# Kernel tuning notes

Hardware: AMD Instinct MI355X
Metric: run time of the kernel (lower is better)

The kernel has to match this reference:

```python
import jax, jax.numpy as jnp
import numpy as np

HID = 1024  # hidden size of the bilinear interaction space

def setup_inputs() -> dict:
    key = jax.random.key(0)
    k1, k2, kw1, kb1, kw2, kwo, kbo = jax.random.split(key, 7)
    B, N1, N2, D1, D2, OUT = 4, 128, 128, 768, 768, 2
    s1 = 1.0 / np.sqrt(D1)
    s2 = 1.0 / np.sqrt(D2)
    so = 1.0 / np.sqrt(HID)
    return {
        "input1": jax.random.normal(k1, (B, N1, D1), dtype=jnp.float32),
        "input2": jax.random.normal(k2, (B, N2, D2), dtype=jnp.float32),
        # torch nn.Linear convention: weight [out, in], y = x @ W.T + b
        "W1": jax.random.uniform(kw1, (HID, D1), jnp.float32, -s1, s1),
        "b1": jax.random.uniform(kb1, (HID,), jnp.float32, -s1, s1),
        "W2": jax.random.uniform(kw2, (HID, D2), jnp.float32, -s2, s2),  # bias=False
        "Wo": jax.random.uniform(kwo, (OUT, HID), jnp.float32, -so, so),
        "bo": jax.random.uniform(kbo, (OUT,), jnp.float32, -so, so),
    }

def reference(input1, input2, W1, b1, W2, Wo, bo):
    # in1: [B, N1, HID], in2: [B, N2, HID]
    in1 = jnp.einsum("bnd,hd->bnh", input1, W1) + b1
    in2 = jnp.einsum("bmd,hd->bmh", input2, W2)
    # broadcast outer-sum -> [B, N1, N2, HID], ReLU, then project to OUT
    h = jax.nn.relu(in1[:, :, None, :] + in2[:, None, :, :])
    return jnp.einsum("bnmh,oh->bnmo", h, Wo) + bo
```

## Files before the change

kernel.cpp:

```cpp
#include <hip/hip_runtime.h>
#include <hip/hip_bf16.h>


typedef __attribute__((ext_vector_type(8))) short s16x8;
typedef __attribute__((ext_vector_type(4))) float f32x4;

#define KP 2304
#define BK 64
#define KHALF 1152
#define NSTEP (KHALF / BK)

__device__ __forceinline__ void gl_lds16(const void* g, void* l) {
    __builtin_amdgcn_global_load_lds(
        (const __attribute__((address_space(1))) unsigned int*)g,
        (__attribute__((address_space(3))) unsigned int*)l, 16, 0, 0);
}

__global__ __launch_bounds__(256) void prepack(
    const float* __restrict__ in1, const float* __restrict__ in2,
    const float* __restrict__ W1, const float* __restrict__ W2,
    ushort* __restrict__ Abig, ushort* __restrict__ Wbig)
{
    const int gid = blockIdx.x * 256 + threadIdx.x;
    const int src = gid / 196608;
    const int rem = gid % 196608;
    const int row = rem / 192;
    const int k4  = (rem % 192) * 4;
    const float* sp;
    ushort* dst;
    if (src == 0) {
        sp  = (row < 512) ? in1 + (size_t)row * 768 + k4
                          : in2 + (size_t)(row - 512) * 768 + k4;
        dst = Abig + (size_t)row * KP + k4;
    } else {
        sp  = (src == 1 ? W1 : W2) + (size_t)row * 768 + k4;
        dst = Wbig + (size_t)(src - 1) * (1024 * KP) + (size_t)row * KP + k4;
    }
    const float4 x = *(const float4*)sp;
    const float xf[4] = {x.x, x.y, x.z, x.w};
    ushort h[4], l[4];
    #pragma unroll
    for (int i = 0; i < 4; ++i) {
        const float v = xf[i];
        __hip_bfloat16 bh = __float2bfloat16(v);
        const float fh = __bfloat162float(bh);
        __hip_bfloat16 bl = __float2bfloat16(v - fh);
        h[i] = *(ushort*)&bh;
        l[i] = *(ushort*)&bl;
    }
    const ushort4 H = make_ushort4(h[0], h[1], h[2], h[3]);
    const ushort4 L = make_ushort4(l[0], l[1], l[2], l[3]);
    if (src == 0) {
        *(ushort4*)(dst)        = H;
        *(ushort4*)(dst + 768)  = L;
        *(ushort4*)(dst + 1536) = H;
    } else {
        *(ushort4*)(dst)        = H;
        *(ushort4*)(dst + 768)  = H;
        *(ushort4*)(dst + 1536) = L;
    }
}

__global__ __launch_bounds__(512) void gemm_mfma(
    const ushort* __restrict__ Abig, const ushort* __restrict__ Wbig,
    const float* __restrict__ b1, float* __restrict__ hid)
{
    const int t    = threadIdx.x;
    const int lane = t & 63;
    const int w    = t >> 6;
    const int kh   = w >> 2;
    const int ws   = w & 3;
    const int row0 = blockIdx.y * 64;
    const int col0 = blockIdx.x * 64;

    const char* __restrict__ A = (const char*)(Abig + (size_t)row0 * KP);
    const char* __restrict__ W = (const char*)(Wbig
                                   + (row0 < 512 ? (size_t)0 : (size_t)1024 * KP)
                                   + (size_t)col0 * KP);

    __shared__ ushort lds[2][2][2][4096];

    const int srow = t >> 3;
    const int kbyt = (((t & 7) ^ (srow & 7)) << 4);
    const size_t rowoff = (size_t)srow * (KP * 2);

    const int wr = ws >> 1, wc = ws & 1;
    const int l15 = lane & 15, kg = lane >> 4;
    int aoff[2][2], boff[2][2];
    #pragma unroll
    for (int kk = 0; kk < 2; ++kk)
        #pragma unroll
        for (int f = 0; f < 2; ++f) {
            const int r = wr * 32 + f * 16 + l15;
            const int c = wc * 32 + f * 16 + l15;
            const int sw_ = kk * 64 + kg * 16;
            aoff[kk][f] = r * 128 + (sw_ ^ ((r & 7) << 4));
            boff[kk][f] = c * 128 + (sw_ ^ ((c & 7) << 4));
        }

#define STAGE(buf, ktk) do {                                                   \
        const size_t kby = (size_t)(ktk) * (BK * 2);                           \
        _Pragma("unroll")                                                      \
        for (int p = 0; p < 4; ++p) {                                          \
            const char* src = (p & 1) ? W : A;                                 \
            const size_t off = rowoff + (size_t)(p >> 1) * (KHALF * 2)         \
                               + kby + kbyt;                                   \
            gl_lds16(src + off,                                                \
                     (char*)&lds[buf][p >> 1][p & 1][0] + t * 16);             \
        }                                                                      \
    } while (0)

    const f32x4 zero = {0.f, 0.f, 0.f, 0.f};
    f32x4 acc[2][2] = {{zero, zero}, {zero, zero}};

    STAGE(0, 0);
    int cur = 0;
    for (int kt = 0; kt < NSTEP; ++kt) {
        asm volatile("s_waitcnt vmcnt(0)" ::: "memory");
        __syncthreads();
        if (kt + 1 < NSTEP) STAGE(cur ^ 1, kt + 1);
        const char* __restrict__ ab = (const char*)&lds[cur][kh][0][0];
        const char* __restrict__ wb = (const char*)&lds[cur][kh][1][0];
        #pragma unroll
        for (int kk = 0; kk < 2; ++kk) {
            s16x8 af[2], bf_[2];
            #pragma unroll
            for (int f = 0; f < 2; ++f) {
                af[f]  = *(const s16x8*)(ab + aoff[kk][f]);
                bf_[f] = *(const s16x8*)(wb + boff[kk][f]);
            }
            #pragma unroll
            for (int fr = 0; fr < 2; ++fr)
                #pragma unroll
                for (int fc = 0; fc < 2; ++fc)
                    acc[fr][fc] = __builtin_amdgcn_mfma_f32_16x16x32_bf16(
                        af[fr], bf_[fc], acc[fr][fc], 0, 0, 0);
        }
        cur ^= 1;
    }
#undef STAGE

    __syncthreads();
    float* red = (float*)&lds[0][0][0][0];
    if (kh == 1) {
        #pragma unroll
        for (int fr = 0; fr < 2; ++fr)
            #pragma unroll
            for (int fc = 0; fc < 2; ++fc)
                *(f32x4*)&red[(((ws * 2 + fr) * 2 + fc) * 64 + lane) * 4] =
                    acc[fr][fc];
    }
    __syncthreads();
    if (kh == 0) {
        float bias[2] = {0.f, 0.f};
        if (row0 < 512) {
            bias[0] = b1[col0 + wc * 32 + l15];
            bias[1] = b1[col0 + wc * 32 + 16 + l15];
        }
        #pragma unroll
        for (int fr = 0; fr < 2; ++fr)
            #pragma unroll
            for (int fc = 0; fc < 2; ++fc) {
                const f32x4 o = *(const f32x4*)
                    &red[(((ws * 2 + fr) * 2 + fc) * 64 + lane) * 4];
                #pragma unroll
                for (int i = 0; i < 4; ++i) {
                    const int r = row0 + wr * 32 + fr * 16 + kg * 4 + i;
                    const int c = col0 + wc * 32 + fc * 16 + l15;
                    hid[(size_t)r * 1024 + c] = acc[fr][fc][i] + o[i] + bias[fc];
                }
            }
    }
}

__global__ __launch_bounds__(256) void pair_kernel(
    const float* __restrict__ hid, const float* __restrict__ Wo,
    const float* __restrict__ bo, float* __restrict__ out)
{
    const int t  = threadIdx.x;
    const int b  = blockIdx.z;
    const int n0 = blockIdx.y * 16;
    const int m0 = blockIdx.x * 16;

    __shared__ float s1[2][16][132];
    __shared__ float s2[2][16][132];
    __shared__ float sw[2][1024];

    #pragma unroll
    for (int q = 0; q < 2; ++q) {
        const int fi = q * 256 + t;
        ((float4*)sw)[fi] = ((const float4*)Wo)[fi];
    }

    const int rr0 = t >> 5;
    const int cc  = (t & 31) << 2;
    const float* __restrict__ base1 = hid + ((size_t)(b * 128 + n0)) * 1024;
    const float* __restrict__ base2 = hid + ((size_t)(512 + b * 128 + m0)) * 1024;

    float4 a0 = *(const float4*)&base1[(size_t)rr0 * 1024 + cc];
    float4 a1 = *(const float4*)&base1[(size_t)(rr0 + 8) * 1024 + cc];
    float4 c0 = *(const float4*)&base2[(size_t)rr0 * 1024 + cc];
    float4 c1 = *(const float4*)&base2[(size_t)(rr0 + 8) * 1024 + cc];

    const int i = t >> 4, j = t & 15;
    float acc0 = 0.f, acc1 = 0.f;
    int cur = 0;

    for (int hc = 0; hc < 8; ++hc) {
        *(float4*)&s1[cur][rr0][cc]     = a0;
        *(float4*)&s1[cur][rr0 + 8][cc] = a1;
        *(float4*)&s2[cur][rr0][cc]     = c0;
        *(float4*)&s2[cur][rr0 + 8][cc] = c1;
        __syncthreads();
        if (hc < 7) {
            const int off = (hc + 1) * 128 + cc;
            a0 = *(const float4*)&base1[(size_t)rr0 * 1024 + off];
            a1 = *(const float4*)&base1[(size_t)(rr0 + 8) * 1024 + off];
            c0 = *(const float4*)&base2[(size_t)rr0 * 1024 + off];
            c1 = *(const float4*)&base2[(size_t)(rr0 + 8) * 1024 + off];
        }
        const float* __restrict__ xrow = &s1[cur][i][0];
        const float* __restrict__ yrow = &s2[cur][j][0];
        const float* __restrict__ u = &sw[0][hc * 128];
        const float* __restrict__ v = &sw[1][hc * 128];
        #pragma unroll
        for (int c4 = 0; c4 < 32; ++c4) {
            const float4 x = *(const float4*)&xrow[c4 * 4];
            const float4 y = *(const float4*)&yrow[c4 * 4];
            const float4 uu = *(const float4*)&u[c4 * 4];
            const float4 vv = *(const float4*)&v[c4 * 4];
            float r;
            r = fmaxf(x.x + y.x, 0.f); acc0 = fmaf(r, uu.x, acc0); acc1 = fmaf(r, vv.x, acc1);
            r = fmaxf(x.y + y.y, 0.f); acc0 = fmaf(r, uu.y, acc0); acc1 = fmaf(r, vv.y, acc1);
            r = fmaxf(x.z + y.z, 0.f); acc0 = fmaf(r, uu.z, acc0); acc1 = fmaf(r, vv.z, acc1);
            r = fmaxf(x.w + y.w, 0.f); acc0 = fmaf(r, uu.w, acc0); acc1 = fmaf(r, vv.w, acc1);
        }
        __syncthreads();
        cur ^= 1;
    }

    const float2 ob = *(const float2*)bo;
    const size_t P = (((size_t)b * 128 + n0 + i) * 128 + (m0 + j)) * 2;
    *(float2*)&out[P] = make_float2(acc0 + ob.x, acc1 + ob.y);
}

extern "C" void kernel_launch(void* const* d_in, const int* in_sizes, int n_in,
                              void* d_out, int out_size, void* d_ws, size_t ws_size,
                              hipStream_t stream) {
    (void)in_sizes; (void)n_in; (void)out_size; (void)ws_size;
    const float* input1 = (const float*)d_in[0];
    const float* input2 = (const float*)d_in[1];
    const float* W1     = (const float*)d_in[2];
    const float* b1     = (const float*)d_in[3];
    const float* W2     = (const float*)d_in[4];
    const float* Wo     = (const float*)d_in[5];
    const float* bo     = (const float*)d_in[6];
    float* out = (float*)d_out;

    ushort* Abig = (ushort*)d_ws;
    ushort* Wbig = Abig + (size_t)1024 * KP;
    float*  hid  = (float*)(Wbig + (size_t)2 * 1024 * KP);

    prepack<<<2304, 256, 0, stream>>>(input1, input2, W1, W2, Abig, Wbig);
    gemm_mfma<<<dim3(16, 16), 512, 0, stream>>>(Abig, Wbig, b1, hid);
    pair_kernel<<<dim3(8, 8, 4), 256, 0, stream>>>(hid, Wo, bo, out);
}
```

Before: 109.2 us.

## Split pair kernel over hidden dimension with atomic accumulation for more blocks

```diff
diff --git a/kernel.cpp b/kernel.cpp
--- a/kernel.cpp
+++ b/kernel.cpp
@@ -173,75 +173,66 @@
     }
 }
 
+__global__ __launch_bounds__(256) void out_init(
+    const float* __restrict__ bo, float* __restrict__ out)
+{
+    const int g = blockIdx.x * 256 + threadIdx.x;
+    *(float2*)&out[(size_t)g * 2] = make_float2(bo[0], bo[1]);
+}
+
 __global__ __launch_bounds__(256) void pair_kernel(
     const float* __restrict__ hid, const float* __restrict__ Wo,
-    const float* __restrict__ bo, float* __restrict__ out)
+    float* __restrict__ out)
 {
     const int t  = threadIdx.x;
-    const int b  = blockIdx.z;
+    const int b  = blockIdx.z >> 2;
+    const int h0 = (blockIdx.z & 3) * 256;
     const int n0 = blockIdx.y * 16;
     const int m0 = blockIdx.x * 16;
 
-    __shared__ float s1[2][16][132];
-    __shared__ float s2[2][16][132];
-    __shared__ float sw[2][1024];
+    __shared__ float s1[16][260];
+    __shared__ float s2[16][260];
+    __shared__ float sw[2][256];
+
+    const float* __restrict__ base1 = hid + ((size_t)(b * 128 + n0)) * 1024 + h0;
+    const float* __restrict__ base2 = hid + ((size_t)(512 + b * 128 + m0)) * 1024 + h0;
 
     #pragma unroll
-    for (int q = 0; q < 2; ++q) {
-        const int fi = q * 256 + t;
-        ((float4*)sw)[fi] = ((const float4*)Wo)[fi];
-    }
-
-    const int rr0 = t >> 5;
-    const int cc  = (t & 31) << 2;
-    const float* __restrict__ base1 = hid + ((size_t)(b * 128 + n0)) * 1024;
-    const float* __restrict__ base2 = hid + ((size_t)(512 + b * 128 + m0)) * 1024;
-
-    float4 a0 = *(const float4*)&base1[(size_t)rr0 * 1024 + cc];
-    float4 a1 = *(const float4*)&base1[(size_t)(rr0 + 8) * 1024 + cc];
-    float4 c0 = *(const float4*)&base2[(size_t)rr0 * 1024 + cc];
-    float4 c1 = *(const float4*)&base2[(size_t)(rr0 + 8) * 1024 + cc];
+    for (int p = 0; p < 4; ++p) {
+        const int slot = p * 256 + t;
+        const int r  = slot >> 6;
+        const int c  = (slot & 63) << 2;
+        *(float4*)&s1[r][c] = *(const float4*)&base1[(size_t)r * 1024 + c];
+        *(float4*)&s2[r][c] = *(const float4*)&base2[(size_t)r * 1024 + c];
+    }
+    if (t < 128) {
+        const int o = t >> 6;
+        const int c = (t & 63) << 2;
+        *(float4*)&sw[o][c] = *(const float4*)&Wo[(size_t)o * 1024 + h0 + c];
+    }
+    __syncthreads();
 
     const int i = t >> 4, j = t & 15;
+    const float* __restrict__ xrow = &s1[i][0];
+    const float* __restrict__ yrow = &s2[j][0];
     float acc0 = 0.f, acc1 = 0.f;
-    int cur = 0;
-
-    for (int hc = 0; hc < 8; ++hc) {
-        *(float4*)&s1[cur][rr0][cc]     = a0;
-        *(float4*)&s1[cur][rr0 + 8][cc] = a1;
-        *(float4*)&s2[cur][rr0][cc]     = c0;
-        *(float4*)&s2[cur][rr0 + 8][cc] = c1;
-        __syncthreads();
-        if (hc < 7) {
-            const int off = (hc + 1) * 128 + cc;
-            a0 = *(const float4*)&base1[(size_t)rr0 * 1024 + off];
-            a1 = *(const float4*)&base1[(size_t)(rr0 + 8) * 1024 + off];
-            c0 = *(const float4*)&base2[(size_t)rr0 * 1024 + off];
-            c1 = *(const float4*)&base2[(size_t)(rr0 + 8) * 1024 + off];
-        }
-        const float* __restrict__ xrow = &s1[cur][i][0];
-        const float* __restrict__ yrow = &s2[cur][j][0];
-        const float* __restrict__ u = &sw[0][hc * 128];
-        const float* __restrict__ v = &sw[1][hc * 128];
-        #pragma unroll
-        for (int c4 = 0; c4 < 32; ++c4) {
-            const float4 x = *(const float4*)&xrow[c4 * 4];
-            const float4 y = *(const float4*)&yrow[c4 * 4];
-            const float4 uu = *(const float4*)&u[c4 * 4];
-            const float4 vv = *(const float4*)&v[c4 * 4];
-            float r;
-            r = fmaxf(x.x + y.x, 0.f); acc0 = fmaf(r, uu.x, acc0); acc1 = fmaf(r, vv.x, acc1);
-            r = fmaxf(x.y + y.y, 0.f); acc0 = fmaf(r, uu.y, acc0); acc1 = fmaf(r, vv.y, acc1);
-            r = fmaxf(x.z + y.z, 0.f); acc0 = fmaf(r, uu.z, acc0); acc1 = fmaf(r, vv.z, acc1);
-            r = fmaxf(x.w + y.w, 0.f); acc0 = fmaf(r, uu.w, acc0); acc1 = fmaf(r, vv.w, acc1);
-        }
-        __syncthreads();
-        cur ^= 1;
-    }
-
-    const float2 ob = *(const float2*)bo;
+
+    #pragma unroll 8
+    for (int c4 = 0; c4 < 64; ++c4) {
+        const float4 x  = *(const float4*)&xrow[c4 * 4];
+        const float4 y  = *(const float4*)&yrow[c4 * 4];
+        const float4 uu = *(const float4*)&sw[0][c4 * 4];
+        const float4 vv = *(const float4*)&sw[1][c4 * 4];
+        float r;
+        r = fmaxf(x.x + y.x, 0.f); acc0 = fmaf(r, uu.x, acc0); acc1 = fmaf(r, vv.x, acc1);
+        r = fmaxf(x.y + y.y, 0.f); acc0 = fmaf(r, uu.y, acc0); acc1 = fmaf(r, vv.y, acc1);
+        r = fmaxf(x.z + y.z, 0.f); acc0 = fmaf(r, uu.z, acc0); acc1 = fmaf(r, vv.z, acc1);
+        r = fmaxf(x.w + y.w, 0.f); acc0 = fmaf(r, uu.w, acc0); acc1 = fmaf(r, vv.w, acc1);
+    }
+
     const size_t P = (((size_t)b * 128 + n0 + i) * 128 + (m0 + j)) * 2;
-    *(float2*)&out[P] = make_float2(acc0 + ob.x, acc1 + ob.y);
+    atomicAdd(&out[P],     acc0);
+    atomicAdd(&out[P + 1], acc1);
 }
 
 extern "C" void kernel_launch(void* const* d_in, const int* in_sizes, int n_in,
@@ -263,5 +254,6 @@
 
     prepack<<<2304, 256, 0, stream>>>(input1, input2, W1, W2, Abig, Wbig);
     gemm_mfma<<<dim3(16, 16), 512, 0, stream>>>(Abig, Wbig, b1, hid);
-    pair_kernel<<<dim3(8, 8, 4), 256, 0, stream>>>(hid, Wo, bo, out);
-}
+    out_init<<<256, 256, 0, stream>>>(bo, out);
+    pair_kernel<<<dim3(8, 8, 16), 256, 0, stream>>>(hid, Wo, out);
+}
```

Measured after the change: 105.9 us. 1.03x faster.
